# Kernel optimization log

Hardware: AMD Instinct MI355X
Metric: run time of the kernel (lower is better)

The kernel has to match this reference:

```python
import jax, jax.numpy as jnp
import numpy as np

B, N, C, H = 32, 4096, 96, 192  # H = dim * mlp_ratio
EPS = 1e-5


def setup_inputs() -> dict:
    key = jax.random.key(0)
    ks = jax.random.split(key, 8)
    s = 0.05  # keep activations numerically tame (module uses scale=0.02 init)
    return {
        "x": jax.random.normal(ks[0], (B, N, C), dtype=jnp.float32),
        "w1": jax.random.normal(ks[1], (H, C), dtype=jnp.float32) * s,
        "bn1_gamma": jnp.ones((H,), jnp.float32),
        "bn1_beta": jnp.zeros((H,), jnp.float32),
        "bn1_mean": jnp.zeros((H,), jnp.float32),
        "bn1_var": jnp.ones((H,), jnp.float32),
        "r": jax.random.normal(ks[2], (H, H), dtype=jnp.float32) * s,
        "i": jax.random.normal(ks[3], (H, H), dtype=jnp.float32) * s,
        "rb": jax.random.normal(ks[4], (H,), dtype=jnp.float32) * s,
        "ib": jax.random.normal(ks[5], (H,), dtype=jnp.float32) * s,
        "w2": jax.random.normal(ks[6], (C, H), dtype=jnp.float32) * s,
        "bn2_gamma": jnp.ones((C,), jnp.float32),
        "bn2_beta": jnp.zeros((C,), jnp.float32),
        "bn2_mean": jnp.zeros((C,), jnp.float32),
        "bn2_var": jnp.ones((C,), jnp.float32),
    }


def _bn(v, gamma, beta, mean, var):
    # inference-mode BatchNorm1d applied over last (channel) dim
    return (v - mean) * (gamma / jnp.sqrt(var + EPS)) + beta


def reference(x, w1, bn1_gamma, bn1_beta, bn1_mean, bn1_var,
              r, i, rb, ib,
              w2, bn2_gamma, bn2_beta, bn2_mean, bn2_var):
    # fc1: 1x1 Conv1d (== per-token linear) + BN + ReLU  -> [B, N, H]
    h = jnp.einsum('bnc,hc->bnh', x, w1)
    h = jax.nn.relu(_bn(h, bn1_gamma, bn1_beta, bn1_mean, bn1_var))
    # FFT over temporal axis (norm='ortho')
    X = jnp.fft.fft(h, axis=1, norm='ortho')
    # torch.einsum('bnc,cc->bnc', x, r) takes the diagonal of r -> elementwise scale
    rd = jnp.diagonal(r)
    idg = jnp.diagonal(i)
    xr = jax.nn.relu(X.real * rd - X.imag * idg + rb)
    xi = jax.nn.relu(X.imag * rd + X.real * idg + ib)
    y = jnp.fft.ifft(xr + 1j * xi, axis=1, norm='ortho').real.astype(jnp.float32)
    # fc2: 1x1 Conv1d + BN -> [B, N, C]
    o = jnp.einsum('bnh,ch->bnc', y, w2)
    return _bn(o, bn2_gamma, bn2_beta, bn2_mean, bn2_var)
```

## Files before the change

### kernel.cpp

```cpp
#include <hip/hip_runtime.h>
#include <stdint.h>
#include <math.h>

#define EPS 1e-5f

typedef __attribute__((ext_vector_type(8))) short bf16x8;
typedef __attribute__((ext_vector_type(4))) float f32x4;
typedef __attribute__((ext_vector_type(2))) float f32x2;

__device__ __forceinline__ unsigned short f2bf(float f) {
    unsigned u = __float_as_uint(f);
    unsigned r = (u + 0x7FFFu + ((u >> 16) & 1u)) >> 16;
    return (unsigned short)r;
}
__device__ __forceinline__ float bf2f(unsigned short h) {
    return __uint_as_float(((unsigned)h) << 16);
}

__device__ __forceinline__ f32x2 mk2(float x, float y) { f32x2 r; r.x = x; r.y = y; return r; }
__device__ __forceinline__ f32x2 irot(f32x2 a) { return mk2(-a.y, a.x); }
__device__ __forceinline__ f32x2 cmulk(f32x2 a, float c, float s) {
    f32x2 as = mk2(-a.y, a.x);
    return a * mk2(c, c) + as * mk2(s, s);
}
__device__ __forceinline__ f32x2 cmulv(f32x2 a, f32x2 b) {
    f32x2 as = mk2(-a.y, a.x);
    return a * mk2(b.x, b.x) + as * mk2(b.y, b.y);
}
__device__ __forceinline__ f32x2 max0(f32x2 a) {
    return mk2(fmaxf(a.x, 0.f), fmaxf(a.y, 0.f));
}

__global__ __launch_bounds__(256) void prep_w_kernel(
    const float* __restrict__ w1, const float* __restrict__ w2,
    unsigned short* __restrict__ w1b, unsigned short* __restrict__ w2b)
{
    int i = blockIdx.x * 256 + threadIdx.x;
    w1b[i] = f2bf(w1[i]);
    w2b[i] = f2bf(w2[i]);
}

__global__ __launch_bounds__(256, 2) void gemm1_kernel(
    const float* __restrict__ x,
    const unsigned short* __restrict__ w1b,
    const float* __restrict__ g1, const float* __restrict__ be1,
    const float* __restrict__ mu1, const float* __restrict__ va1,
    unsigned short* __restrict__ ht)
{
    __shared__ unsigned short ws2[12][192][8];
    __shared__ unsigned short xs2[12][128][8];
    __shared__ float sb[2][192];

    const int tid = threadIdx.x;
    const int T0 = blockIdx.x * 128;
    const int b  = T0 >> 12;
    const int n0 = T0 & 4095;
    const int lane = tid & 63, wid = tid >> 6;
    const int lm = lane & 15, lg = lane >> 4;

    if (tid < 192) {
        float s = g1[tid] * rsqrtf(va1[tid] + EPS);
        sb[0][tid] = s;
        sb[1][tid] = be1[tid] - mu1[tid] * s;
    }
    #pragma unroll
    for (int i = 0; i < 9; ++i) {
        int id = tid + i * 256;
        int ch = id / 12, c8 = (id % 12) * 8;
        *(uint4*)&ws2[c8 >> 3][ch][0] = *(const uint4*)(w1b + (size_t)ch * 96 + c8);
    }
    const float* xb = x + (size_t)T0 * 96;
    #pragma unroll
    for (int i = 0; i < 12; ++i) {
        int id = tid + i * 256;
        int t = id / 24, c4 = (id % 24) * 4;
        float4 v = *(const float4*)(xb + (size_t)t * 96 + c4);
        ushort4 hv = { f2bf(v.x), f2bf(v.y), f2bf(v.z), f2bf(v.w) };
        *(ushort4*)&xs2[c4 >> 3][t][c4 & 7] = hv;
    }
    __syncthreads();

    const int t0w = wid * 32;
    f32x4 acc[12][2];
    #pragma unroll
    for (int f = 0; f < 12; ++f)
        #pragma unroll
        for (int nf = 0; nf < 2; ++nf) acc[f][nf] = (f32x4){0.f, 0.f, 0.f, 0.f};

    #pragma unroll
    for (int ks = 0; ks < 3; ++ks) {
        const int g = ks * 4 + lg;
        bf16x8 bfrag[2];
        #pragma unroll
        for (int nf = 0; nf < 2; ++nf)
            bfrag[nf] = *(const bf16x8*)&xs2[g][t0w + nf * 16 + lm][0];
        #pragma unroll
        for (int f = 0; f < 12; ++f) {
            bf16x8 afrag = *(const bf16x8*)&ws2[g][f * 16 + lm][0];
            acc[f][0] = __builtin_amdgcn_mfma_f32_16x16x32_bf16(afrag, bfrag[0], acc[f][0], 0, 0, 0);
            acc[f][1] = __builtin_amdgcn_mfma_f32_16x16x32_bf16(afrag, bfrag[1], acc[f][1], 0, 0, 0);
        }
    }

    unsigned short* hb = ht + (size_t)b * 192 * 4096 + n0;
    #pragma unroll
    for (int f = 0; f < 12; ++f) {
        #pragma unroll
        for (int r = 0; r < 4; ++r) {
            int hc = f * 16 + lg * 4 + r;
            float s = sb[0][hc], bb = sb[1][hc];
            #pragma unroll
            for (int nf = 0; nf < 2; ++nf) {
                float v = fmaxf(fmaf(acc[f][nf][r], s, bb), 0.f);
                hb[(size_t)hc * 4096 + t0w + nf * 16 + lm] = f2bf(v);
            }
        }
    }
}

#define NBIDX(k) ((((k) & 0x0FF0)) | (((k) ^ ((k) >> 4)) & 0x0F))

template <int S>
__device__ __forceinline__ void dft16(f32x2 v[16]) {
    const float C1 = 0.92387953251128675613f;
    const float S1 = 0.38268343236508977173f;
    const float R  = 0.70710678118654752440f;
    const float sg = (float)S;
    f32x2 g[16];
    #pragma unroll
    for (int a1 = 0; a1 < 4; ++a1) {
        f32x2 v0 = v[a1], v1 = v[a1 + 4], v2 = v[a1 + 8], v3 = v[a1 + 12];
        f32x2 t0 = v0 + v2, t1 = v0 - v2;
        f32x2 t2 = v1 + v3, t3 = v1 - v3;
        f32x2 u = irot(t3);
        g[0 * 4 + a1] = t0 + t2;
        g[1 * 4 + a1] = (S > 0) ? (t1 + u) : (t1 - u);
        g[2 * 4 + a1] = t0 - t2;
        g[3 * 4 + a1] = (S > 0) ? (t1 - u) : (t1 + u);
    }
    g[4 + 1]  = cmulk(g[4 + 1],  C1,  sg * S1);
    g[4 + 2]  = cmulk(g[4 + 2],  R,   sg * R);
    g[4 + 3]  = cmulk(g[4 + 3],  S1,  sg * C1);
    g[8 + 1]  = cmulk(g[8 + 1],  R,   sg * R);
    {
        f32x2 a = g[8 + 2];
        g[8 + 2] = (S > 0) ? irot(a) : mk2(a.y, -a.x);
    }
    g[8 + 3]  = cmulk(g[8 + 3],  -R,  sg * R);
    g[12 + 1] = cmulk(g[12 + 1], S1,  sg * C1);
    g[12 + 2] = cmulk(g[12 + 2], -R,  sg * R);
    g[12 + 3] = cmulk(g[12 + 3], -C1, -sg * S1);
    #pragma unroll
    for (int r1 = 0; r1 < 4; ++r1) {
        f32x2 v0 = g[r1 * 4 + 0], v1 = g[r1 * 4 + 1],
              v2 = g[r1 * 4 + 2], v3 = g[r1 * 4 + 3];
        f32x2 t0 = v0 + v2, t1 = v0 - v2;
        f32x2 t2 = v1 + v3, t3 = v1 - v3;
        f32x2 u = irot(t3);
        v[r1 + 0]  = t0 + t2;
        v[r1 + 4]  = (S > 0) ? (t1 + u) : (t1 - u);
        v[r1 + 8]  = t0 - t2;
        v[r1 + 12] = (S > 0) ? (t1 - u) : (t1 + u);
    }
}

__device__ __forceinline__ void twiddle_ladder(f32x2 w, f32x2 W[16]) {
    W[1] = w;
    W[2] = cmulv(W[1], W[1]);
    W[3] = cmulv(W[2], W[1]);
    W[4] = cmulv(W[2], W[2]);
    W[5] = cmulv(W[4], W[1]);
    W[6] = cmulv(W[4], W[2]);
    W[7] = cmulv(W[4], W[3]);
    W[8] = cmulv(W[4], W[4]);
    #pragma unroll
    for (int j = 1; j < 8; ++j) W[8 + j] = cmulv(W[8], W[j]);
}

template <int S>
__device__ __forceinline__ void fft4096_ip(f32x2* __restrict__ SB, int tid)
{
    const float TWO_PI = 6.28318530717958647692f;
    f32x2 v[16];
    {
        const int ii = (tid & 0xF0) | ((tid ^ (tid >> 4)) & 0x0F);
        #pragma unroll
        for (int a = 0; a < 16; ++a) v[a] = SB[a * 256 + ii];
        dft16<S>(v);
        float c0, s0;
        __sincosf((float)S * TWO_PI * (float)tid * (1.f / 4096.f), &s0, &c0);
        f32x2 W[16];
        twiddle_ladder(mk2(c0, s0), W);
        #pragma unroll
        for (int r2 = 1; r2 < 16; ++r2) v[r2] = cmulv(v[r2], W[r2]);
        __syncthreads();
        #pragma unroll
        for (int r2 = 0; r2 < 16; ++r2) SB[r2 * 256 + tid] = v[r2];
    }
    __syncthreads();
    const int r = tid >> 4, t1 = tid & 15;
    {
        #pragma unroll
        for (int t2 = 0; t2 < 16; ++t2) v[t2] = SB[r * 256 + t2 * 16 + t1];
        dft16<S>(v);
        float c0, s0;
        __sincosf((float)S * TWO_PI * (float)t1 * (1.f / 256.f), &s0, &c0);
        f32x2 W[16];
        twiddle_ladder(mk2(c0, s0), W);
        #pragma unroll
        for (int m = 1; m < 16; ++m) v[m] = cmulv(v[m], W[m]);
        __syncthreads();
        #pragma unroll
        for (int m = 0; m < 16; ++m) SB[r * 256 + m * 16 + (t1 ^ m)] = v[m];
    }
    __syncthreads();
    {
        const int m = tid & 15;
        #pragma unroll
        for (int q = 0; q < 16; ++q) v[q] = SB[r * 256 + m * 16 + (q ^ m)];
        dft16<S>(v);
        const int inner = (m * 16) | ((r ^ m) & 15);
        __syncthreads();
        #pragma unroll
        for (int p = 0; p < 16; ++p) SB[p * 256 + inner] = v[p];
    }
    __syncthreads();
}

__global__ __launch_bounds__(256) void fft_mid_kernel(
    unsigned short* __restrict__ ht,
    const float* __restrict__ rmat,
    const float* __restrict__ imat,
    const float* __restrict__ rb,
    const float* __restrict__ ib)
{
    __shared__ f32x2 SB[4096];

    const int tid = threadIdx.x;
    const int pp  = blockIdx.x;
    const int b   = blockIdx.y;
    const int h1  = 2 * pp, h2 = 2 * pp + 1;
    unsigned short* row1 = ht + ((size_t)b * 192 + h1) * 4096;
    unsigned short* row2 = ht + ((size_t)b * 192 + h2) * 4096;

    #pragma unroll
    for (int i = 0; i < 2; ++i) {
        int nb = i * 2048 + tid * 8;
        uint4 v1 = *(const uint4*)(row1 + nb);
        uint4 v2 = *(const uint4*)(row2 + nb);
        const unsigned short* p1 = (const unsigned short*)&v1;
        const unsigned short* p2 = (const unsigned short*)&v2;
        int a = nb >> 8;
        #pragma unroll
        for (int j = 0; j < 8; ++j) {
            int t = (nb + j) & 255;
            int ii = (t & 0xF0) | ((t ^ (t >> 4)) & 0x0F);
            SB[a * 256 + ii] = mk2(bf2f(p1[j]), bf2f(p2[j]));
        }
    }
    __syncthreads();

    fft4096_ip<-1>(SB, tid);

    const f32x2 RD = mk2(rmat[(size_t)h1 * 192 + h1], rmat[(size_t)h2 * 192 + h2]);
    const f32x2 IG = mk2(imat[(size_t)h1 * 192 + h1], imat[(size_t)h2 * 192 + h2]);
    const f32x2 RB = mk2(rb[h1], rb[h2]);
    const f32x2 IB = mk2(ib[h1], ib[h2]);

    for (int k = tid; k <= 2048; k += 256) {
        int m = (4096 - k) & 4095;
        f32x2 Fk = SB[NBIDX(k)], Fm = SB[NBIDX(m)];
        const float sc = 1.f / 128.f;
        f32x2 P = mk2(Fk.x + Fm.x, Fk.y + Fm.y) * mk2(sc, sc);
        f32x2 Q = mk2(Fk.y - Fm.y, Fm.x - Fk.x) * mk2(sc, sc);
        f32x2 Zkr = max0(P * RD - Q * IG + RB);
        f32x2 Zki = max0(Q * RD + P * IG + IB);
        f32x2 Zmr = max0(P * RD + Q * IG + RB);
        f32x2 Zmi = max0(P * IG - Q * RD + IB);
        float A = Zkr.x + Zmr.x, Bv = Zki.y - Zmi.y;
        float C = Zki.x - Zmi.x, D = Zkr.y + Zmr.y;
        SB[NBIDX(k)] = mk2(0.5f * (A - Bv), 0.5f * (C + D));
        SB[NBIDX(m)] = mk2(0.5f * (A + Bv), 0.5f * (D - C));
    }
    __syncthreads();

    fft4096_ip<1>(SB, tid);

    const float inv = 1.f / 64.f;
    #pragma unroll
    for (int i = 0; i < 2; ++i) {
        int nb = i * 2048 + tid * 8;
        uint4 v1, v2;
        unsigned short* p1 = (unsigned short*)&v1;
        unsigned short* p2 = (unsigned short*)&v2;
        int a = nb >> 8;
        #pragma unroll
        for (int j = 0; j < 8; ++j) {
            int t = (nb + j) & 255;
            int ii = (t & 0xF0) | ((t ^ (t >> 4)) & 0x0F);
            f32x2 g = SB[a * 256 + ii];
            p1[j] = f2bf(g.x * inv);
            p2[j] = f2bf(g.y * inv);
        }
        *(uint4*)(row1 + nb) = v1;
        *(uint4*)(row2 + nb) = v2;
    }
}

__global__ __launch_bounds__(256, 2) void gemm2_kernel(
    const unsigned short* __restrict__ ht,
    const unsigned short* __restrict__ w2b,
    const float* __restrict__ g2, const float* __restrict__ be2,
    const float* __restrict__ mu2, const float* __restrict__ va2,
    float* __restrict__ out)
{
    __shared__ unsigned short at[64][208];
    __shared__ unsigned short w2s[96][200];

    const int tid = threadIdx.x;
    const int T0 = blockIdx.x * 64;
    const int b  = T0 >> 12;
    const int n0 = T0 & 4095;
    const int lane = tid & 63, wid = tid >> 6;
    const int lm = lane & 15, lg = lane >> 4;

    #pragma unroll
    for (int i = 0; i < 9; ++i) {
        int id = tid + i * 256;
        int ch = id / 24, k8 = (id % 24) * 8;
        *(uint4*)&w2s[ch][k8] = *(const uint4*)(w2b + (size_t)ch * 192 + k8);
    }
    const unsigned short* src = ht + (size_t)b * 192 * 4096 + n0;
    #pragma unroll
    for (int i = 0; i < 3; ++i) {
        int pid = tid + i * 256;
        int hc0 = (pid >> 3) * 2, t8 = (pid & 7) * 8;
        uint4 v0 = *(const uint4*)(src + (size_t)hc0 * 4096 + t8);
        uint4 v1 = *(const uint4*)(src + (size_t)(hc0 + 1) * 4096 + t8);
        const unsigned short* p0 = (const unsigned short*)&v0;
        const unsigned short* p1 = (const unsigned short*)&v1;
        #pragma unroll
        for (int u = 0; u < 8; ++u) {
            *(unsigned*)&at[t8 + u][hc0] = (unsigned)p0[u] | ((unsigned)p1[u] << 16);
        }
    }
    __syncthreads();

    f32x4 acc[6];
    #pragma unroll
    for (int nf = 0; nf < 6; ++nf) acc[nf] = (f32x4){0.f, 0.f, 0.f, 0.f};

    #pragma unroll
    for (int ks = 0; ks < 6; ++ks) {
        const int k0 = ks * 32 + lg * 8;
        bf16x8 afrag = *(const bf16x8*)&at[wid * 16 + lm][k0];
        #pragma unroll
        for (int nf = 0; nf < 6; ++nf) {
            bf16x8 bfv = *(const bf16x8*)&w2s[nf * 16 + lm][k0];
            acc[nf] = __builtin_amdgcn_mfma_f32_16x16x32_bf16(afrag, bfv, acc[nf], 0, 0, 0);
        }
    }

    float* ob = out + (size_t)T0 * 96;
    #pragma unroll
    for (int nf = 0; nf < 6; ++nf) {
        int ch = nf * 16 + lm;
        float s  = g2[ch] * rsqrtf(va2[ch] + EPS);
        float bb = be2[ch] - mu2[ch] * s;
        int tokb = wid * 16 + lg * 4;
        #pragma unroll
        for (int r = 0; r < 4; ++r) {
            ob[(size_t)(tokb + r) * 96 + ch] = fmaf(acc[nf][r], s, bb);
        }
    }
}

extern "C" void kernel_launch(void* const* d_in, const int* in_sizes, int n_in,
                              void* d_out, int out_size, void* d_ws, size_t ws_size,
                              hipStream_t stream)
{
    const float* x   = (const float*)d_in[0];
    const float* w1  = (const float*)d_in[1];
    const float* g1  = (const float*)d_in[2];
    const float* be1 = (const float*)d_in[3];
    const float* mu1 = (const float*)d_in[4];
    const float* va1 = (const float*)d_in[5];
    const float* r   = (const float*)d_in[6];
    const float* im  = (const float*)d_in[7];
    const float* rb  = (const float*)d_in[8];
    const float* ib  = (const float*)d_in[9];
    const float* w2  = (const float*)d_in[10];
    const float* g2  = (const float*)d_in[11];
    const float* be2 = (const float*)d_in[12];
    const float* mu2 = (const float*)d_in[13];
    const float* va2 = (const float*)d_in[14];
    float* out = (float*)d_out;

    unsigned short* ht  = (unsigned short*)d_ws;
    unsigned short* w1b = ht + (size_t)32 * 192 * 4096;
    unsigned short* w2b = w1b + 192 * 96;

    prep_w_kernel<<<dim3(72), 256, 0, stream>>>(w1, w2, w1b, w2b);
    gemm1_kernel<<<dim3(1024), 256, 0, stream>>>(x, w1b, g1, be1, mu1, va1, ht);
    fft_mid_kernel<<<dim3(96, 32), 256, 0, stream>>>(ht, r, im, rb, ib);
    gemm2_kernel<<<dim3(2048), 256, 0, stream>>>(ht, w2b, g2, be2, mu2, va2, out);
}
```

Baseline: 96.48 us.

## Store FFT shared-memory buffer as packed fp16 and drop wave-local barriers

The FFT kernel's shared buffer now holds each complex pair as packed fp16 (converted with round-toward-zero) instead of two float32 values. This halves LDS footprint and traffic per block, which can allow more resident blocks and cheaper LDS accesses. Several __syncthreads are replaced by scheduling barriers where the in-place read and write sets stay inside one wavefront. The cost is extra pack and unpack conversions and reduced precision and range of the intermediate FFT values, which could add numerical error or overflow for large magnitudes.

```diff
diff --git a/kernel.cpp b/kernel.cpp
--- a/kernel.cpp
+++ b/kernel.cpp
@@ -7,6 +7,7 @@
 typedef __attribute__((ext_vector_type(8))) short bf16x8;
 typedef __attribute__((ext_vector_type(4))) float f32x4;
 typedef __attribute__((ext_vector_type(2))) float f32x2;
+typedef __attribute__((ext_vector_type(2))) __fp16 fp16x2;
 
 __device__ __forceinline__ unsigned short f2bf(float f) {
     unsigned u = __float_as_uint(f);
@@ -29,6 +30,14 @@
 }
 __device__ __forceinline__ f32x2 max0(f32x2 a) {
     return mk2(fmaxf(a.x, 0.f), fmaxf(a.y, 0.f));
+}
+__device__ __forceinline__ unsigned pk16(f32x2 v) {
+    fp16x2 h = __builtin_amdgcn_cvt_pkrtz(v.x, v.y);
+    return *(unsigned*)&h;
+}
+__device__ __forceinline__ f32x2 up16(unsigned u) {
+    fp16x2 h = *(fp16x2*)&u;
+    return mk2((float)h.x, (float)h.y);
 }
 
 __global__ __launch_bounds__(256) void prep_w_kernel(
@@ -178,14 +187,14 @@
 }
 
 template <int S>
-__device__ __forceinline__ void fft4096_ip(f32x2* __restrict__ SB, int tid)
+__device__ __forceinline__ void fft4096_ip(unsigned* __restrict__ SB, int tid)
 {
     const float TWO_PI = 6.28318530717958647692f;
     f32x2 v[16];
     {
         const int ii = (tid & 0xF0) | ((tid ^ (tid >> 4)) & 0x0F);
         #pragma unroll
-        for (int a = 0; a < 16; ++a) v[a] = SB[a * 256 + ii];
+        for (int a = 0; a < 16; ++a) v[a] = up16(SB[a * 256 + ii]);
         dft16<S>(v);
         float c0, s0;
         __sincosf((float)S * TWO_PI * (float)tid * (1.f / 4096.f), &s0, &c0);
@@ -193,15 +202,15 @@
         twiddle_ladder(mk2(c0, s0), W);
         #pragma unroll
         for (int r2 = 1; r2 < 16; ++r2) v[r2] = cmulv(v[r2], W[r2]);
-        __syncthreads();
-        #pragma unroll
-        for (int r2 = 0; r2 < 16; ++r2) SB[r2 * 256 + tid] = v[r2];
+        __builtin_amdgcn_sched_barrier(0);
+        #pragma unroll
+        for (int r2 = 0; r2 < 16; ++r2) SB[r2 * 256 + tid] = pk16(v[r2]);
     }
     __syncthreads();
     const int r = tid >> 4, t1 = tid & 15;
     {
         #pragma unroll
-        for (int t2 = 0; t2 < 16; ++t2) v[t2] = SB[r * 256 + t2 * 16 + t1];
+        for (int t2 = 0; t2 < 16; ++t2) v[t2] = up16(SB[r * 256 + t2 * 16 + t1]);
         dft16<S>(v);
         float c0, s0;
         __sincosf((float)S * TWO_PI * (float)t1 * (1.f / 256.f), &s0, &c0);
@@ -209,20 +218,20 @@
         twiddle_ladder(mk2(c0, s0), W);
         #pragma unroll
         for (int m = 1; m < 16; ++m) v[m] = cmulv(v[m], W[m]);
-        __syncthreads();
-        #pragma unroll
-        for (int m = 0; m < 16; ++m) SB[r * 256 + m * 16 + (t1 ^ m)] = v[m];
-    }
-    __syncthreads();
+        __builtin_amdgcn_sched_barrier(0);
+        #pragma unroll
+        for (int m = 0; m < 16; ++m) SB[r * 256 + m * 16 + (t1 ^ m)] = pk16(v[m]);
+    }
+    __builtin_amdgcn_sched_barrier(0);
     {
         const int m = tid & 15;
         #pragma unroll
-        for (int q = 0; q < 16; ++q) v[q] = SB[r * 256 + m * 16 + (q ^ m)];
+        for (int q = 0; q < 16; ++q) v[q] = up16(SB[r * 256 + m * 16 + (q ^ m)]);
         dft16<S>(v);
         const int inner = (m * 16) | ((r ^ m) & 15);
         __syncthreads();
         #pragma unroll
-        for (int p = 0; p < 16; ++p) SB[p * 256 + inner] = v[p];
+        for (int p = 0; p < 16; ++p) SB[p * 256 + inner] = pk16(v[p]);
     }
     __syncthreads();
 }
@@ -234,7 +243,7 @@
     const float* __restrict__ rb,
     const float* __restrict__ ib)
 {
-    __shared__ f32x2 SB[4096];
+    __shared__ unsigned SB[4096];
 
     const int tid = threadIdx.x;
     const int pp  = blockIdx.x;
@@ -255,7 +264,7 @@
         for (int j = 0; j < 8; ++j) {
             int t = (nb + j) & 255;
             int ii = (t & 0xF0) | ((t ^ (t >> 4)) & 0x0F);
-            SB[a * 256 + ii] = mk2(bf2f(p1[j]), bf2f(p2[j]));
+            SB[a * 256 + ii] = pk16(mk2(bf2f(p1[j]), bf2f(p2[j])));
         }
     }
     __syncthreads();
@@ -269,7 +278,7 @@
 
     for (int k = tid; k <= 2048; k += 256) {
         int m = (4096 - k) & 4095;
-        f32x2 Fk = SB[NBIDX(k)], Fm = SB[NBIDX(m)];
+        f32x2 Fk = up16(SB[NBIDX(k)]), Fm = up16(SB[NBIDX(m)]);
         const float sc = 1.f / 128.f;
         f32x2 P = mk2(Fk.x + Fm.x, Fk.y + Fm.y) * mk2(sc, sc);
         f32x2 Q = mk2(Fk.y - Fm.y, Fm.x - Fk.x) * mk2(sc, sc);
@@ -279,8 +288,8 @@
         f32x2 Zmi = max0(P * IG - Q * RD + IB);
         float A = Zkr.x + Zmr.x, Bv = Zki.y - Zmi.y;
         float C = Zki.x - Zmi.x, D = Zkr.y + Zmr.y;
-        SB[NBIDX(k)] = mk2(0.5f * (A - Bv), 0.5f * (C + D));
-        SB[NBIDX(m)] = mk2(0.5f * (A + Bv), 0.5f * (D - C));
+        SB[NBIDX(k)] = pk16(mk2(0.5f * (A - Bv), 0.5f * (C + D)));
+        SB[NBIDX(m)] = pk16(mk2(0.5f * (A + Bv), 0.5f * (D - C)));
     }
     __syncthreads();
 
@@ -298,7 +307,7 @@
         for (int j = 0; j < 8; ++j) {
             int t = (nb + j) & 255;
             int ii = (t & 0xF0) | ((t ^ (t >> 4)) & 0x0F);
-            f32x2 g = SB[a * 256 + ii];
+            f32x2 g = up16(SB[a * 256 + ii]);
             p1[j] = f2bf(g.x * inv);
             p2[j] = f2bf(g.y * inv);
         }
```

After: 98.34 us. No clear change (+1.9%).

## Hoist FFT twiddle ladders and drop intra-wave block barriers in FFT stages

Applied to the files above, without the earlier changes.

Both 4096-point FFTs now share twiddle factors computed once per thread before the forward pass. The inverse reuses them through a conjugating complex multiply instead of recomputing sincos and the power ladder. Several __syncthreads between stages are replaced by scheduling barriers, on the basis that each thread's reads and writes in those stages stay inside its own 64-lane wave. This cuts transcendental and ladder work and block-wide stalls, but it relies on wave-synchronous LDS ordering and keeps 32 more twiddle registers live, which adds register pressure.

```diff
diff --git a/kernel.cpp b/kernel.cpp
--- a/kernel.cpp
+++ b/kernel.cpp
@@ -26,6 +26,14 @@
 __device__ __forceinline__ f32x2 cmulv(f32x2 a, f32x2 b) {
     f32x2 as = mk2(-a.y, a.x);
     return a * mk2(b.x, b.x) + as * mk2(b.y, b.y);
+}
+__device__ __forceinline__ f32x2 cmulvc(f32x2 a, f32x2 b) {
+    f32x2 as = mk2(a.y, -a.x);
+    return a * mk2(b.x, b.x) + as * mk2(b.y, b.y);
+}
+template <int S>
+__device__ __forceinline__ f32x2 cmulT(f32x2 a, f32x2 b) {
+    return (S < 0) ? cmulv(a, b) : cmulvc(a, b);
 }
 __device__ __forceinline__ f32x2 max0(f32x2 a) {
     return mk2(fmaxf(a.x, 0.f), fmaxf(a.y, 0.f));
@@ -178,22 +186,18 @@
 }
 
 template <int S>
-__device__ __forceinline__ void fft4096_ip(f32x2* __restrict__ SB, int tid)
-{
-    const float TWO_PI = 6.28318530717958647692f;
+__device__ __forceinline__ void fft4096_ip(f32x2* __restrict__ SB, int tid,
+                                           const f32x2 WA[16], const f32x2 WB[16])
+{
     f32x2 v[16];
     {
         const int ii = (tid & 0xF0) | ((tid ^ (tid >> 4)) & 0x0F);
         #pragma unroll
         for (int a = 0; a < 16; ++a) v[a] = SB[a * 256 + ii];
         dft16<S>(v);
-        float c0, s0;
-        __sincosf((float)S * TWO_PI * (float)tid * (1.f / 4096.f), &s0, &c0);
-        f32x2 W[16];
-        twiddle_ladder(mk2(c0, s0), W);
-        #pragma unroll
-        for (int r2 = 1; r2 < 16; ++r2) v[r2] = cmulv(v[r2], W[r2]);
-        __syncthreads();
+        #pragma unroll
+        for (int r2 = 1; r2 < 16; ++r2) v[r2] = cmulT<S>(v[r2], WA[r2]);
+        __builtin_amdgcn_sched_barrier(0);
         #pragma unroll
         for (int r2 = 0; r2 < 16; ++r2) SB[r2 * 256 + tid] = v[r2];
     }
@@ -203,17 +207,13 @@
         #pragma unroll
         for (int t2 = 0; t2 < 16; ++t2) v[t2] = SB[r * 256 + t2 * 16 + t1];
         dft16<S>(v);
-        float c0, s0;
-        __sincosf((float)S * TWO_PI * (float)t1 * (1.f / 256.f), &s0, &c0);
-        f32x2 W[16];
-        twiddle_ladder(mk2(c0, s0), W);
-        #pragma unroll
-        for (int m = 1; m < 16; ++m) v[m] = cmulv(v[m], W[m]);
-        __syncthreads();
+        #pragma unroll
+        for (int m = 1; m < 16; ++m) v[m] = cmulT<S>(v[m], WB[m]);
+        __builtin_amdgcn_sched_barrier(0);
         #pragma unroll
         for (int m = 0; m < 16; ++m) SB[r * 256 + m * 16 + (t1 ^ m)] = v[m];
     }
-    __syncthreads();
+    __builtin_amdgcn_sched_barrier(0);
     {
         const int m = tid & 15;
         #pragma unroll
@@ -258,9 +258,19 @@
             SB[a * 256 + ii] = mk2(bf2f(p1[j]), bf2f(p2[j]));
         }
     }
-    __syncthreads();
-
-    fft4096_ip<-1>(SB, tid);
+
+    const float TWO_PI = 6.28318530717958647692f;
+    f32x2 WA[16], WB[16];
+    {
+        float c0, s0;
+        __sincosf(-TWO_PI * (float)tid * (1.f / 4096.f), &s0, &c0);
+        twiddle_ladder(mk2(c0, s0), WA);
+        __sincosf(-TWO_PI * (float)(tid & 15) * (1.f / 256.f), &s0, &c0);
+        twiddle_ladder(mk2(c0, s0), WB);
+    }
+    __syncthreads();
+
+    fft4096_ip<-1>(SB, tid, WA, WB);
 
     const f32x2 RD = mk2(rmat[(size_t)h1 * 192 + h1], rmat[(size_t)h2 * 192 + h2]);
     const f32x2 IG = mk2(imat[(size_t)h1 * 192 + h1], imat[(size_t)h2 * 192 + h2]);
@@ -284,7 +294,7 @@
     }
     __syncthreads();
 
-    fft4096_ip<1>(SB, tid);
+    fft4096_ip<1>(SB, tid, WA, WB);
 
     const float inv = 1.f / 64.f;
     #pragma unroll
```

Result: slower. 105.9 us (+9.8%).
